# Kernel optimization log

Hardware: AMD Instinct MI355X
Metric: run time of the kernel (lower is better)

The kernel has to match this reference:

```python
import jax, jax.numpy as jnp
import numpy as np

LOOKBACK = 1
LOOKAHEAD = 0
SEQ, BATCH, IN, HID = 1024, 16, 1024, 1024
K = LOOKBACK + 1 + LOOKAHEAD


def quick_gelu(x):
    return x * jax.nn.sigmoid(1.702 * x)


def setup_inputs() -> dict:
    key = jax.random.key(0)
    ks = jax.random.split(key, 5)
    scale = 1.0 / np.sqrt(IN * K)  # like torch Conv1d default init scale
    X = jax.random.normal(ks[0], (SEQ, BATCH, IN), dtype=jnp.float32)
    Wz = jax.random.normal(ks[1], (HID, IN, K), dtype=jnp.float32) * scale
    bz = jax.random.normal(ks[2], (HID,), dtype=jnp.float32) * scale
    Wf = jax.random.normal(ks[3], (HID, IN, K), dtype=jnp.float32) * scale
    bf = jax.random.normal(ks[4], (HID,), dtype=jnp.float32) * scale
    return {"X": X, "Wz": Wz, "bz": bz, "Wf": Wf, "bf": bf}


def _conv1d(x_pad, W, b):
    # x_pad: (B, Cin, T+K-1), W: (Cout, Cin, K) -> (B, Cout, T)
    y = jax.lax.conv_general_dilated(
        x_pad, W, window_strides=(1,), padding="VALID",
        dimension_numbers=("NCH", "OIH", "NCH"))
    return y + b[None, :, None]


def reference(X, Wz, bz, Wf, bf):
    # pad time dim: lookback zeros before, lookahead zeros after
    X_pad = jnp.pad(X, ((LOOKBACK, LOOKAHEAD), (0, 0), (0, 0)))
    X_pad = jnp.transpose(X_pad, (1, 2, 0))  # (B, Cin, T+K-1)
    Z = jnp.transpose(_conv1d(X_pad, Wz, bz), (2, 0, 1))  # (T, B, H)
    F = jnp.transpose(_conv1d(X_pad, Wf, bf), (2, 0, 1))  # (T, B, H)
    Z = quick_gelu(Z)
    F = jax.nn.sigmoid(F)

    def step(h, fz):
        f, z = fz
        h = f * z + (1.0 - f) * h
        return h, h

    h0 = jnp.zeros((BATCH, HID), dtype=X.dtype)
    _, H = jax.lax.scan(step, h0, (F, Z))  # H: (T, B, HID)
    return H, H[-1:, :, :]
```

## Files before the change

kernel.cpp:

```cpp
#include <hip/hip_runtime.h>
#include <stdint.h>

#define T_SEQ 1024
#define B_SZ  16
#define C_IN  1024
#define C_HID 1024
#define M_ROWS (T_SEQ * B_SZ)
#define N_COLS (2 * C_HID)
#define K_DIM  (2 * C_IN)

#define NCHUNK 64
#define CLEN   (T_SEQ / NCHUNK)
#define NBH    (B_SZ * C_HID)

typedef __attribute__((ext_vector_type(8))) short bf16x8;
typedef __attribute__((ext_vector_type(4))) float f32x4;
typedef unsigned short u16;

#define MFMA __builtin_amdgcn_mfma_f32_16x16x32_bf16

__device__ __forceinline__ u16 f2bf(float f) {
  union { float f; unsigned u; } v; v.f = f;
  unsigned r = v.u + 0x7fffu + ((v.u >> 16) & 1u);
  return (u16)(r >> 16);
}
__device__ __forceinline__ float bf2f(unsigned s) {
  union { unsigned u; float f; } v; v.u = s << 16;
  return v.f;
}

__device__ __forceinline__ void async_cp16(const u16* g, u16* l) {
  __builtin_amdgcn_global_load_lds(
      (const __attribute__((address_space(1))) unsigned*)(uintptr_t)g,
      (__attribute__((address_space(3))) unsigned*)(uintptr_t)l,
      16, 0, 0);
}

__global__ __launch_bounds__(256) void k_prep(const float* __restrict__ X,
                                              const float* __restrict__ Wz,
                                              const float* __restrict__ Wf,
                                              u16* __restrict__ Xp,
                                              u16* __restrict__ Wt) {
  int blk = blockIdx.x;
  if (blk < 16400) {
    int i = blk * 256 + threadIdx.x;
    const int total4 = (M_ROWS + B_SZ) * C_IN / 4;
    if (i >= total4) return;
    int e = i << 2;
    const int PAD = B_SZ * C_IN;
    ushort4 o;
    if (e < PAD) {
      o.x = o.y = o.z = o.w = 0;
    } else {
      float4 v = *reinterpret_cast<const float4*>(X + (e - PAD));
      o.x = f2bf(v.x); o.y = f2bf(v.y); o.z = f2bf(v.z); o.w = f2bf(v.w);
    }
    *reinterpret_cast<ushort4*>(Xp + e) = o;
  } else {
    int i = (blk - 16400) * 256 + threadIdx.x;
    if (i >= 2 * 1024 * 1024) return;
    int g  = i >> 20;
    int hc = i & ((1 << 20) - 1);
    int h  = hc >> 10;
    int c  = hc & 1023;
    const float* W = g ? Wf : Wz;
    float2 w = *reinterpret_cast<const float2*>(W + ((size_t)(h << 10) + c) * 2);
    size_t n = ((size_t)h << 1) | (size_t)g;
    Wt[n * K_DIM + c]        = f2bf(w.x);
    Wt[n * K_DIM + 1024 + c] = f2bf(w.y);
  }
}

__global__ __launch_bounds__(512, 2) void k_gemm8(const u16* __restrict__ Xp,
                                                  const u16* __restrict__ Wt,
                                                  const float* __restrict__ bz,
                                                  const float* __restrict__ bfv,
                                                  u16* __restrict__ Cb) {
  __shared__ u16 lds[2][2][2][8192];
  const int tid  = threadIdx.x;
  const int lane = tid & 63;
  const int wid  = tid >> 6;
  const int wr = wid >> 2;
  const int wc = wid & 3;
  const int lr = lane & 15;

  int wg = (blockIdx.x & 7) * 64 + (blockIdx.x >> 3);
  const int m0 = (wg >> 3) << 8;
  const int n0 = (wg & 7) << 8;

  const int p    = tid << 4;
  const int q    = p ^ (((p >> 7) & 7) << 4);
  const int grow = q >> 7;
  const int gcol = (q & 127) >> 1;
  const int ldsw = (tid >> 6) << 9;

  const int rbase = lr << 6;
  int co[2];
#pragma unroll
  for (int ks = 0; ks < 2; ++ks)
    co[ks] = ((((ks << 6) | ((lane >> 4) << 4)) ^ ((lr & 7) << 4)) >> 1);

  auto stage = [&](int j) {
    int kt = j >> 2, part = j & 3, buf = kt & 1;
    if (part >= 2) {
      int h = part - 2;
      const u16* g = Xp + (size_t)(m0 + (h << 7) + grow + ((kt >= 16) ? B_SZ : 0)) * C_IN
                        + ((kt & 15) << 6) + gcol;
      u16* l = &lds[buf][0][h][ldsw];
      async_cp16(g, l);
      async_cp16(g + (size_t)64 * C_IN, l + 4096);
    } else {
      const u16* g = Wt + (size_t)(n0 + (part << 7) + grow) * K_DIM + (kt << 6) + gcol;
      u16* l = &lds[buf][1][part][ldsw];
      async_cp16(g, l);
      async_cp16(g + (size_t)64 * K_DIM, l + 4096);
    }
  };

  f32x4 acc[8][4] = {};
  bf16x8 a[4][2], b0[2][2], b1[2][2];

  for (int j = 0; j < 7; ++j) stage(j);
  asm volatile("s_waitcnt vmcnt(6)" ::: "memory");
  __builtin_amdgcn_s_barrier();

#pragma unroll 2
  for (int t = 0; t < 32; ++t) {
    const int buf = t & 1;
    const u16* pA = &lds[buf][0][wr][0];
    const u16* pB = &lds[buf][1][wc >> 1][(wc & 1) << 12];
    const int jb = 4 * t + 7;

#pragma unroll
    for (int mi = 0; mi < 4; ++mi)
#pragma unroll
      for (int ks = 0; ks < 2; ++ks)
        a[mi][ks] = *(const bf16x8*)(pA + (mi << 10) + rbase + co[ks]);
#pragma unroll
    for (int ni = 0; ni < 2; ++ni)
#pragma unroll
      for (int ks = 0; ks < 2; ++ks)
        b0[ni][ks] = *(const bf16x8*)(pB + (ni << 10) + rbase + co[ks]);
    if (jb < 128) stage(jb);
    __builtin_amdgcn_s_barrier();
    asm volatile("s_waitcnt lgkmcnt(0)" ::: "memory");
    __builtin_amdgcn_s_setprio(1);
#pragma unroll
    for (int mi = 0; mi < 4; ++mi)
#pragma unroll
      for (int ni = 0; ni < 2; ++ni)
#pragma unroll
        for (int ks = 0; ks < 2; ++ks)
          acc[mi][ni] = MFMA(a[mi][ks], b0[ni][ks], acc[mi][ni], 0, 0, 0);
    __builtin_amdgcn_s_setprio(0);
    __builtin_amdgcn_s_barrier();

#pragma unroll
    for (int ni = 0; ni < 2; ++ni)
#pragma unroll
      for (int ks = 0; ks < 2; ++ks)
        b1[ni][ks] = *(const bf16x8*)(pB + ((2 + ni) << 10) + rbase + co[ks]);
    if (jb + 1 < 128) stage(jb + 1);
    __builtin_amdgcn_s_barrier();
    asm volatile("s_waitcnt lgkmcnt(0)" ::: "memory");
    __builtin_amdgcn_s_setprio(1);
#pragma unroll
    for (int mi = 0; mi < 4; ++mi)
#pragma unroll
      for (int ni = 0; ni < 2; ++ni)
#pragma unroll
        for (int ks = 0; ks < 2; ++ks)
          acc[mi][2 + ni] = MFMA(a[mi][ks], b1[ni][ks], acc[mi][2 + ni], 0, 0, 0);
    __builtin_amdgcn_s_setprio(0);
    __builtin_amdgcn_s_barrier();

#pragma unroll
    for (int mi = 0; mi < 4; ++mi)
#pragma unroll
      for (int ks = 0; ks < 2; ++ks)
        a[mi][ks] = *(const bf16x8*)(pA + ((4 + mi) << 10) + rbase + co[ks]);
    if (jb + 2 < 128) stage(jb + 2);
    __builtin_amdgcn_s_barrier();
    asm volatile("s_waitcnt lgkmcnt(0)" ::: "memory");
    __builtin_amdgcn_s_setprio(1);
#pragma unroll
    for (int mi = 0; mi < 4; ++mi)
#pragma unroll
      for (int ni = 0; ni < 2; ++ni)
#pragma unroll
        for (int ks = 0; ks < 2; ++ks)
          acc[4 + mi][2 + ni] = MFMA(a[mi][ks], b1[ni][ks], acc[4 + mi][2 + ni], 0, 0, 0);
    __builtin_amdgcn_s_setprio(0);
    __builtin_amdgcn_s_barrier();

    if (jb + 3 < 128) stage(jb + 3);
    if (t < 30) asm volatile("s_waitcnt vmcnt(6)" ::: "memory");
    else        asm volatile("s_waitcnt vmcnt(0)" ::: "memory");
    __builtin_amdgcn_s_barrier();
    __builtin_amdgcn_s_setprio(1);
#pragma unroll
    for (int mi = 0; mi < 4; ++mi)
#pragma unroll
      for (int ni = 0; ni < 2; ++ni)
#pragma unroll
        for (int ks = 0; ks < 2; ++ks)
          acc[4 + mi][ni] = MFMA(a[mi][ks], b0[ni][ks], acc[4 + mi][ni], 0, 0, 0);
    __builtin_amdgcn_s_setprio(0);
    __builtin_amdgcn_s_barrier();
  }

  const int colp = lane & 15;
  const bool isz = (colp & 1) == 0;
  const float kk = isz ? 1.702f : 1.0f;
  const int jj = colp >> 1;
  const int b4 = lane >> 4;
  const int hbase = ((n0 + (wc << 6)) >> 1) + jj;
  const int c    = m0 >> 8;
  const int nfb  = (n0 >> 4) + (wc << 2);
  float* exA = (float*)&lds[0][0][0][0];
  float* exB = exA + 2048;

  uint4 trj[8];
#pragma unroll
  for (int ni = 0; ni < 4; ++ni) {
    float bias = isz ? bz[hbase + 8 * ni] : bfv[hbase + 8 * ni];
    float hh[4] = {0.f, 0.f, 0.f, 0.f}, P[4] = {1.f, 1.f, 1.f, 1.f};
#pragma unroll
    for (int mi = 0; mi < 8; ++mi) {
      unsigned tw[4];
#pragma unroll
      for (int r = 0; r < 4; ++r) {
        float v = acc[mi][ni][r] + bias;
        float s = 1.f / (1.f + __expf(-kk * v));
        float act = isz ? v * s : s;
        float par = __shfl_xor(act, 1, 64);
        float z = isz ? act : par;
        float f = isz ? par : act;
        hh[r] += f * (z - hh[r]);
        P[r]  *= (1.f - f);
        tw[r] = (unsigned)f2bf(hh[r]) | ((unsigned)f2bf(P[r]) << 16);
      }
      if (wr == 0) {
        if (!(lane & 1)) {
          size_t fi = (size_t)((c << 4) + mi) * 128 + nfb + ni;
          uint4 o; o.x = tw[0]; o.y = tw[1]; o.z = tw[2]; o.w = tw[3];
          *reinterpret_cast<uint4*>(Cb + fi * 256 + (b4 << 6) + (jj << 3)) = o;
        }
      } else {
        uint4 o; o.x = tw[0]; o.y = tw[1]; o.z = tw[2]; o.w = tw[3];
        trj[mi] = o;
      }
    }
    const int xi = (((((wc << 2) | b4) << 3) | jj) << 2 | ni) << 2;
    if (wr == 0 && !(lane & 1)) {
#pragma unroll
      for (int r = 0; r < 4; ++r) { exA[xi + r] = hh[r]; exB[xi + r] = P[r]; }
    }
    __syncthreads();
    if (wr == 1 && !(lane & 1)) {
      float A0[4], B0[4];
#pragma unroll
      for (int r = 0; r < 4; ++r) { A0[r] = exA[xi + r]; B0[r] = exB[xi + r]; }
#pragma unroll
      for (int mi = 0; mi < 8; ++mi) {
        uint4 o;
        unsigned* ow = &o.x;
        const unsigned* iw = &trj[mi].x;
#pragma unroll
        for (int r = 0; r < 4; ++r) {
          float hp = bf2f(iw[r] & 0xffffu);
          float pp = bf2f(iw[r] >> 16);
          float H2 = hp + pp * A0[r];
          float P2 = pp * B0[r];
          ow[r] = (unsigned)f2bf(H2) | ((unsigned)f2bf(P2) << 16);
        }
        size_t fi = (size_t)((c << 4) + 8 + mi) * 128 + nfb + ni;
        *reinterpret_cast<uint4*>(Cb + fi * 256 + (b4 << 6) + (jj << 3)) = o;
      }
    }
  }
}

__global__ __launch_bounds__(256) void k_scan(const u16* __restrict__ Cb,
                                              float* __restrict__ out) {
  int i = blockIdx.x * 256 + threadIdx.x;
  int h  = i & (C_HID - 1);
  int b4 = (i >> 10) & 3;
  int c  = i >> 12;
  const size_t lane_off = (size_t)(h >> 3) * 256 + b4 * 64 + (h & 7) * 8;
  float hh[4] = {0.f, 0.f, 0.f, 0.f};
  for (int cc = 0; cc < c; ++cc) {
    uint4 w = *reinterpret_cast<const uint4*>(
        Cb + ((size_t)cc * CLEN + CLEN - 1) * 32768 + lane_off);
    const unsigned* ww = &w.x;
#pragma unroll
    for (int r = 0; r < 4; ++r) {
      float A = bf2f(ww[r] & 0xffffu), B = bf2f(ww[r] >> 16);
      hh[r] = A + B * hh[r];
    }
  }
#pragma unroll 4
  for (int tt = 0; tt < CLEN; ++tt) {
    size_t t = (size_t)c * CLEN + tt;
    uint4 w = *reinterpret_cast<const uint4*>(Cb + t * 32768 + lane_off);
    const unsigned* ww = &w.x;
    float* op = out + t * 16384 + (size_t)b4 * 4096 + h;
#pragma unroll
    for (int r = 0; r < 4; ++r) {
      float v = bf2f(ww[r] & 0xffffu) + bf2f(ww[r] >> 16) * hh[r];
      op[r * 1024] = v;
      if (c == NCHUNK - 1 && tt == CLEN - 1)
        out[(size_t)M_ROWS * C_HID + (size_t)b4 * 4096 + h + r * 1024] = v;
    }
  }
}

extern "C" void kernel_launch(void* const* d_in, const int* in_sizes, int n_in,
                              void* d_out, int out_size, void* d_ws, size_t ws_size,
                              hipStream_t stream) {
  const float* X   = (const float*)d_in[0];
  const float* Wz  = (const float*)d_in[1];
  const float* bz  = (const float*)d_in[2];
  const float* Wf  = (const float*)d_in[3];
  const float* bf_ = (const float*)d_in[4];
  float* out = (float*)d_out;

  u16* Xp = (u16*)d_ws;
  u16* Wt = Xp + (size_t)(M_ROWS + B_SZ) * C_IN;
  u16* Cb = Wt + (size_t)N_COLS * K_DIM;

  hipLaunchKernelGGL(k_prep, dim3(16400 + 8192), dim3(256), 0, stream,
                     X, Wz, Wf, Xp, Wt);
  hipLaunchKernelGGL(k_gemm8, dim3((M_ROWS / 256) * (N_COLS / 256)), dim3(512), 0,
                     stream, Xp, Wt, bz, bf_, Cb);
  hipLaunchKernelGGL(k_scan, dim3(NCHUNK * 4096 / 256), dim3(256), 0, stream,
                     Cb, out);
}
```

Baseline: 297.4 us.

## Software-pipeline LDS fragment loads across MFMA phases and drop intra-loop barriers

Restructures the GEMM main loop so the A and B fragments for the next k-tile are read from LDS into separate registers (aN, b0N, a2) while the current tile's MFMAs run. The fragments for the first tile are preloaded before the loop. Several s_barrier and explicit lgkmcnt(0) waits per iteration are removed, leaving the compiler's own waitcnt insertion to order the LDS reads. This aims to hide LDS latency behind matrix-core work and cut synchronisation stalls, at the cost of higher VGPR pressure and a more delicate correctness argument about buffer reuse.

```diff
diff --git a/kernel.cpp b/kernel.cpp
--- a/kernel.cpp
+++ b/kernel.cpp
@@ -118,11 +118,25 @@
   };
 
   f32x4 acc[8][4] = {};
-  bf16x8 a[4][2], b0[2][2], b1[2][2];
+  bf16x8 a[4][2], a2[4][2], aN[4][2], b0[2][2], b0N[2][2], b1[2][2];
 
   for (int j = 0; j < 7; ++j) stage(j);
   asm volatile("s_waitcnt vmcnt(6)" ::: "memory");
   __builtin_amdgcn_s_barrier();
+  {
+    const u16* pA = &lds[0][0][wr][0];
+    const u16* pB = &lds[0][1][wc >> 1][(wc & 1) << 12];
+#pragma unroll
+    for (int mi = 0; mi < 4; ++mi)
+#pragma unroll
+      for (int ks = 0; ks < 2; ++ks)
+        a[mi][ks] = *(const bf16x8*)(pA + (mi << 10) + rbase + co[ks]);
+#pragma unroll
+    for (int ni = 0; ni < 2; ++ni)
+#pragma unroll
+      for (int ks = 0; ks < 2; ++ks)
+        b0[ni][ks] = *(const bf16x8*)(pB + (ni << 10) + rbase + co[ks]);
+  }
 
 #pragma unroll 2
   for (int t = 0; t < 32; ++t) {
@@ -132,18 +146,11 @@
     const int jb = 4 * t + 7;
 
 #pragma unroll
-    for (int mi = 0; mi < 4; ++mi)
+    for (int ni = 0; ni < 2; ++ni)
 #pragma unroll
       for (int ks = 0; ks < 2; ++ks)
-        a[mi][ks] = *(const bf16x8*)(pA + (mi << 10) + rbase + co[ks]);
-#pragma unroll
-    for (int ni = 0; ni < 2; ++ni)
-#pragma unroll
-      for (int ks = 0; ks < 2; ++ks)
-        b0[ni][ks] = *(const bf16x8*)(pB + (ni << 10) + rbase + co[ks]);
+        b1[ni][ks] = *(const bf16x8*)(pB + ((2 + ni) << 10) + rbase + co[ks]);
     if (jb < 128) stage(jb);
-    __builtin_amdgcn_s_barrier();
-    asm volatile("s_waitcnt lgkmcnt(0)" ::: "memory");
     __builtin_amdgcn_s_setprio(1);
 #pragma unroll
     for (int mi = 0; mi < 4; ++mi)
@@ -156,13 +163,11 @@
     __builtin_amdgcn_s_barrier();
 
 #pragma unroll
-    for (int ni = 0; ni < 2; ++ni)
+    for (int mi = 0; mi < 4; ++mi)
 #pragma unroll
       for (int ks = 0; ks < 2; ++ks)
-        b1[ni][ks] = *(const bf16x8*)(pB + ((2 + ni) << 10) + rbase + co[ks]);
+        a2[mi][ks] = *(const bf16x8*)(pA + ((4 + mi) << 10) + rbase + co[ks]);
     if (jb + 1 < 128) stage(jb + 1);
-    __builtin_amdgcn_s_barrier();
-    asm volatile("s_waitcnt lgkmcnt(0)" ::: "memory");
     __builtin_amdgcn_s_setprio(1);
 #pragma unroll
     for (int mi = 0; mi < 4; ++mi)
@@ -174,14 +179,7 @@
     __builtin_amdgcn_s_setprio(0);
     __builtin_amdgcn_s_barrier();
 
-#pragma unroll
-    for (int mi = 0; mi < 4; ++mi)
-#pragma unroll
-      for (int ks = 0; ks < 2; ++ks)
-        a[mi][ks] = *(const bf16x8*)(pA + ((4 + mi) << 10) + rbase + co[ks]);
     if (jb + 2 < 128) stage(jb + 2);
-    __builtin_amdgcn_s_barrier();
-    asm volatile("s_waitcnt lgkmcnt(0)" ::: "memory");
     __builtin_amdgcn_s_setprio(1);
 #pragma unroll
     for (int mi = 0; mi < 4; ++mi)
@@ -189,7 +187,7 @@
       for (int ni = 0; ni < 2; ++ni)
 #pragma unroll
         for (int ks = 0; ks < 2; ++ks)
-          acc[4 + mi][2 + ni] = MFMA(a[mi][ks], b1[ni][ks], acc[4 + mi][2 + ni], 0, 0, 0);
+          acc[4 + mi][2 + ni] = MFMA(a2[mi][ks], b1[ni][ks], acc[4 + mi][2 + ni], 0, 0, 0);
     __builtin_amdgcn_s_setprio(0);
     __builtin_amdgcn_s_barrier();
 
@@ -197,6 +195,20 @@
     if (t < 30) asm volatile("s_waitcnt vmcnt(6)" ::: "memory");
     else        asm volatile("s_waitcnt vmcnt(0)" ::: "memory");
     __builtin_amdgcn_s_barrier();
+    if (t < 31) {
+      const u16* qA = &lds[buf ^ 1][0][wr][0];
+      const u16* qB = &lds[buf ^ 1][1][wc >> 1][(wc & 1) << 12];
+#pragma unroll
+      for (int mi = 0; mi < 4; ++mi)
+#pragma unroll
+        for (int ks = 0; ks < 2; ++ks)
+          aN[mi][ks] = *(const bf16x8*)(qA + (mi << 10) + rbase + co[ks]);
+#pragma unroll
+      for (int ni = 0; ni < 2; ++ni)
+#pragma unroll
+        for (int ks = 0; ks < 2; ++ks)
+          b0N[ni][ks] = *(const bf16x8*)(qB + (ni << 10) + rbase + co[ks]);
+    }
     __builtin_amdgcn_s_setprio(1);
 #pragma unroll
     for (int mi = 0; mi < 4; ++mi)
@@ -204,9 +216,20 @@
       for (int ni = 0; ni < 2; ++ni)
 #pragma unroll
         for (int ks = 0; ks < 2; ++ks)
-          acc[4 + mi][ni] = MFMA(a[mi][ks], b0[ni][ks], acc[4 + mi][ni], 0, 0, 0);
+          acc[4 + mi][ni] = MFMA(a2[mi][ks], b0[ni][ks], acc[4 + mi][ni], 0, 0, 0);
     __builtin_amdgcn_s_setprio(0);
-    __builtin_amdgcn_s_barrier();
+    if (t < 31) {
+#pragma unroll
+      for (int mi = 0; mi < 4; ++mi)
+#pragma unroll
+        for (int ks = 0; ks < 2; ++ks)
+          a[mi][ks] = aN[mi][ks];
+#pragma unroll
+      for (int ni = 0; ni < 2; ++ni)
+#pragma unroll
+        for (int ks = 0; ks < 2; ++ks)
+          b0[ni][ks] = b0N[ni][ks];
+    }
   }
 
   const int colp = lane & 15;
```

Measured after the change: 393.4 us. 1.32x slower.
